# Kernel optimization log

Measured on AMD Instinct MI355X. Metric: run time of the kernel, lower is better.

Reference implementation:

```python
import jax, jax.numpy as jnp
import numpy as np

N, D, H, L = 50000, 128, 4, 3
E = 800000
C = D // H            # head dim = 32
NEG_SLOPE = 0.2       # PyG GATv2Conv default negative_slope
LN_EPS = 1e-5         # nn.LayerNorm default eps


def setup_inputs() -> dict:
    key = jax.random.key(0)
    ks = jax.random.split(key, 8)
    s = 1.0 / np.sqrt(D).astype(np.float32)
    return {
        "fine_poi_x": jax.random.normal(ks[0], (N, D), jnp.float32),
        "edge_index": jax.random.randint(ks[1], (2, E), 0, N, dtype=jnp.int32),
        "Wl": jax.random.normal(ks[2], (L, D, D), jnp.float32) * s,
        "bl": jnp.zeros((L, D), jnp.float32),
        "Wr": jax.random.normal(ks[3], (L, D, D), jnp.float32) * s,
        "br": jnp.zeros((L, D), jnp.float32),
        "att": jax.random.normal(ks[4], (L, H, C), jnp.float32) * s,
        "bias": jnp.zeros((L, D), jnp.float32),
        "gamma": jnp.ones((L, D), jnp.float32),
        "beta": jnp.zeros((L, D), jnp.float32),
    }


def _gatv2_conv(x, src, dst, Wl, bl, Wr, br, att, bias):
    # x: [N, D]; src/dst: [E'] (self-loops already appended)
    xl = (x @ Wl + bl).reshape(N, H, C)   # source-side transform (lin_l)
    xr = (x @ Wr + br).reshape(N, H, C)   # target-side transform (lin_r)
    m = xl[src] + xr[dst]                 # [E', H, C] per-edge pre-activation
    m = jax.nn.leaky_relu(m, NEG_SLOPE)
    e = jnp.einsum("ehc,hc->eh", m, att)  # [E', H] attention logits
    # segment softmax over edges grouped by destination node
    emax = jax.ops.segment_max(e, dst, num_segments=N)      # [N, H]
    ee = jnp.exp(e - emax[dst])
    denom = jax.ops.segment_sum(ee, dst, num_segments=N)    # [N, H]
    alpha = ee / denom[dst]               # self-loops guarantee denom >= 1 term
    out = jax.ops.segment_sum(xl[src] * alpha[:, :, None], dst, num_segments=N)
    return out.reshape(N, D) + bias


def _layernorm(x, g, b):
    mu = jnp.mean(x, axis=-1, keepdims=True)
    var = jnp.var(x, axis=-1, keepdims=True)
    return (x - mu) * jax.lax.rsqrt(var + LN_EPS) * g + b


def reference(fine_poi_x, edge_index, Wl, bl, Wr, br, att, bias, gamma, beta):
    # PyG GATv2Conv add_self_loops=True: append i->i edges
    loops = jnp.arange(N, dtype=edge_index.dtype)
    src = jnp.concatenate([edge_index[0], loops])
    dst = jnp.concatenate([edge_index[1], loops])
    x = fine_poi_x
    for i in range(L):
        h = _gatv2_conv(x, src, dst, Wl[i], bl[i], Wr[i], br[i], att[i], bias[i])
        x = _layernorm(x + h, gamma[i], beta[i])
        if i != L - 1:
            x = jax.nn.relu(x)
    return x
```

## Files before the change

### kernel.cpp

```cpp
#include <hip/hip_runtime.h>

#define N_NODES 50000
#define N_EDGES 800000
#define DIM 128
#define TOT_EDGES (N_EDGES + N_NODES)
#define LOG2E 1.44269504088896f

#define BSHIFT 9
#define BNODES 512
#define NB ((N_NODES + BNODES - 1) / BNODES)
#define BCAP 16384
#define EPB 4096
#define EPT 16
#define NBLK_A ((TOT_EDGES + EPB - 1) / EPB)

typedef __attribute__((ext_vector_type(8))) _Float16 f16x8;
typedef __attribute__((ext_vector_type(2))) _Float16 h2;
typedef __attribute__((ext_vector_type(4))) float f32x4;
typedef decltype(__builtin_amdgcn_cvt_pkrtz(0.f, 0.f)) fp16v2;

__device__ inline uint h2u(h2 v) { return __builtin_bit_cast(uint, v); }
__device__ inline h2 u2h(uint v) { return __builtin_bit_cast(h2, v); }
__device__ inline uint pk2u(fp16v2 v) { return __builtin_bit_cast(uint, v); }

__device__ inline float rowsum16(float v) {
  int x;
  x = __builtin_amdgcn_update_dpp(0, __float_as_int(v), 0x128, 0xF, 0xF, true);
  v += __int_as_float(x);
  x = __builtin_amdgcn_update_dpp(0, __float_as_int(v), 0x124, 0xF, 0xF, true);
  v += __int_as_float(x);
  x = __builtin_amdgcn_update_dpp(0, __float_as_int(v), 0x122, 0xF, 0xF, true);
  v += __int_as_float(x);
  x = __builtin_amdgcn_update_dpp(0, __float_as_int(v), 0x121, 0xF, 0xF, true);
  v += __int_as_float(x);
  return v;
}

__device__ inline float quadsum4(float v) {
  int x;
  x = __builtin_amdgcn_update_dpp(0, __float_as_int(v), 0xB1, 0xF, 0xF, true);
  v += __int_as_float(x);
  x = __builtin_amdgcn_update_dpp(0, __float_as_int(v), 0x4E, 0xF, 0xF, true);
  v += __int_as_float(x);
  return v;
}


__global__ __launch_bounds__(256) void convx_kernel(const float* __restrict__ x,
                                                    uint* __restrict__ xb,
                                                    int* __restrict__ bcnt) {
  if (blockIdx.x == 0 && threadIdx.x < NB) bcnt[threadIdx.x] = 0;
  int t = blockIdx.x * 256 + threadIdx.x;
  if (t < N_NODES * (DIM / 2)) {
    float2 v = ((const float2*)x)[t];
    xb[t] = pk2u(__builtin_amdgcn_cvt_pkrtz(v.x, v.y));
  }
}

__global__ __launch_bounds__(256) void convwa_kernel(const float* __restrict__ Wl,
                                                     const float* __restrict__ Wr,
                                                     ushort* __restrict__ Wt,
                                                     const float* __restrict__ att,
                                                     uint* __restrict__ attc,
                                                     uint* __restrict__ col) {
  int t = blockIdx.x * 256 + threadIdx.x;
  if (blockIdx.x == 0) {
    int u = threadIdx.x;
    if (u < 192) {
      float a0 = att[2 * u] * LOG2E, a1 = att[2 * u + 1] * LOG2E;
      attc[u] = pk2u(__builtin_amdgcn_cvt_pkrtz(a0, a1));
    }
    if (u < 64) col[TOT_EDGES + u] = 0u;
  }
  if (t >= 3 * 2 * DIM * DIM) return;
  int k = t & 127;
  int n = (t >> 7) & 127;
  int w = (t >> 14) & 1;
  int l = t >> 15;
  const float* W = w ? Wr : Wl;
  _Float16 h = (_Float16)W[l * DIM * DIM + k * DIM + n];
  Wt[t] = __builtin_bit_cast(ushort, h);
}


__global__ __launch_bounds__(256) void partA_kernel(const int* __restrict__ srcArr,
                                                    const int* __restrict__ dstArr,
                                                    int* __restrict__ bcnt,
                                                    uint2* __restrict__ bbuf) {
  int tid = threadIdx.x;
  int e0 = blockIdx.x * EPB;
  __shared__ int hist[NB], base[NB], loff[NB];
  if (tid < NB) { hist[tid] = 0; loff[tid] = 0; }
  __syncthreads();

  int sv[EPT], dv[EPT];
#pragma unroll
  for (int i = 0; i < EPT; ++i) {
    int e = e0 + i * 256 + tid;
    int s = 0, d = -1;
    if (e < TOT_EDGES) {
      if (e < N_EDGES) { s = srcArr[e]; d = dstArr[e]; }
      else { s = e - N_EDGES; d = s; }
    }
    sv[i] = s; dv[i] = d;
    if (d >= 0) atomicAdd(&hist[d >> BSHIFT], 1);
  }
  __syncthreads();
  if (tid < NB) {
    int h = hist[tid];
    if (h > 0) base[tid] = atomicAdd(&bcnt[tid], h);
  }
  __syncthreads();
#pragma unroll
  for (int i = 0; i < EPT; ++i) {
    int d = dv[i];
    if (d >= 0) {
      int b = d >> BSHIFT;
      int p = atomicAdd(&loff[b], 1);
      bbuf[(size_t)b * BCAP + base[b] + p] = make_uint2((uint)sv[i], (uint)d);
    }
  }
}


__global__ __launch_bounds__(512) void partB_kernel(const uint2* __restrict__ bbuf,
                                                    const int* __restrict__ bcnt,
                                                    int* __restrict__ rowptr,
                                                    uint* __restrict__ col) {
  int b = blockIdx.x, tid = threadIdx.x;

  __shared__ int s[128];
  if (tid < 128) s[tid] = (tid < NB) ? bcnt[tid] : 0;
  __syncthreads();
  for (int off = 1; off < 128; off <<= 1) {
    int t = 0;
    if (tid < 128 && tid >= off) t = s[tid - off];
    __syncthreads();
    if (tid < 128) s[tid] += t;
    __syncthreads();
  }
  int cb = (b > 0) ? s[b - 1] : 0;
  int m = bcnt[b];
  if (b == 0 && tid == 0) rowptr[N_NODES] = TOT_EDGES;
  const uint2* buf = bbuf + (size_t)b * BCAP;

  __shared__ int cnt[BNODES], scn[BNODES], cur[BNODES];
  cnt[tid] = 0;
  __syncthreads();
  for (int e = tid; e < m; e += 512) {
    int d = (int)buf[e].y;
    atomicAdd(&cnt[d & (BNODES - 1)], 1);
  }
  __syncthreads();
  int c = cnt[tid];
  scn[tid] = c;
  __syncthreads();
  for (int off = 1; off < BNODES; off <<= 1) {
    int t = (tid >= off) ? scn[tid - off] : 0;
    __syncthreads();
    scn[tid] += t;
    __syncthreads();
  }
  int excl = scn[tid] - c;
  int node = b * BNODES + tid;
  if (node < N_NODES) rowptr[node] = cb + excl;
  cur[tid] = excl;
  __syncthreads();
  for (int e = tid; e < m; e += 512) {
    uint2 sd = buf[e];
    int p = atomicAdd(&cur[(int)sd.y & (BNODES - 1)], 1);
    col[cb + p] = sd.x * 16u;
  }
}


__global__ __launch_bounds__(256) void gemm_mfma_kernel(
    const uint* __restrict__ xb,
    const ushort* __restrict__ Wt,
    const float* __restrict__ bl, const float* __restrict__ br,
    uint* __restrict__ xl, uint* __restrict__ xr) {
  int wave = threadIdx.x >> 6, lane = threadIdx.x & 63;
  int lr = lane & 15, kq = lane >> 4;
  int m0 = blockIdx.x * 64;

  const ushort* W = Wt + (wave >> 1) * (DIM * DIM);
  const float* bias = (wave >> 1) ? br : bl;
  uint* outp = (wave >> 1) ? xr : xl;
  int n0 = (wave & 1) * 64;
  const ushort* xbp = (const ushort*)xb;

  f16x8 bfrag[4][4];
#pragma unroll
  for (int nt = 0; nt < 4; ++nt)
#pragma unroll
    for (int kt = 0; kt < 4; ++kt)
      bfrag[nt][kt] = *(const f16x8*)(W + (n0 + nt * 16 + lr) * DIM + kt * 32 + kq * 8);

  f32x4 acc[4][4];
#pragma unroll
  for (int mt = 0; mt < 4; ++mt)
#pragma unroll
    for (int nt = 0; nt < 4; ++nt)
      acc[mt][nt] = (f32x4){0.f, 0.f, 0.f, 0.f};

  f16x8 af[4];
  {
    int m = m0 + lr;
    int mc = m < N_NODES ? m : N_NODES - 1;
#pragma unroll
    for (int kt = 0; kt < 4; ++kt)
      af[kt] = *(const f16x8*)(xbp + (size_t)mc * DIM + kt * 32 + kq * 8);
  }
#pragma unroll
  for (int mt = 0; mt < 4; ++mt) {
    f16x8 afn[4];
    if (mt < 3) {
      int m2 = m0 + (mt + 1) * 16 + lr;
      int mc2 = m2 < N_NODES ? m2 : N_NODES - 1;
#pragma unroll
      for (int kt = 0; kt < 4; ++kt)
        afn[kt] = *(const f16x8*)(xbp + (size_t)mc2 * DIM + kt * 32 + kq * 8);
    }
#pragma unroll
    for (int nt = 0; nt < 4; ++nt)
#pragma unroll
      for (int kt = 0; kt < 4; ++kt)
        acc[mt][nt] = __builtin_amdgcn_mfma_f32_16x16x32_f16(bfrag[nt][kt], af[kt],
                                                             acc[mt][nt], 0, 0, 0);
    if (mt < 3) {
      af[0] = afn[0]; af[1] = afn[1]; af[2] = afn[2]; af[3] = afn[3];
    }
  }

#pragma unroll
  for (int mt = 0; mt < 4; ++mt) {
    int m = m0 + mt * 16 + lr;
    if (m < N_NODES) {
#pragma unroll
      for (int nt = 0; nt < 4; ++nt) {
        int n = n0 + nt * 16 + kq * 4;
        float4 bb = *(const float4*)(bias + n);
        uint2 o;
        o.x = pk2u(__builtin_amdgcn_cvt_pkrtz(acc[mt][nt][0] + bb.x, acc[mt][nt][1] + bb.y));
        o.y = pk2u(__builtin_amdgcn_cvt_pkrtz(acc[mt][nt][2] + bb.z, acc[mt][nt][3] + bb.w));
        *(uint2*)(outp + (size_t)m * (DIM / 2) + (n >> 1)) = o;
      }
    }
  }
}


__global__ __launch_bounds__(64) void att_kernel(
    const uint4* __restrict__ xinb, const uint4* __restrict__ xlb,
    const uint4* __restrict__ xrb, const int* __restrict__ rowptr,
    const uint* __restrict__ col, const uint4* __restrict__ attc,
    const float4* __restrict__ bias, const float4* __restrict__ gamma,
    const float4* __restrict__ beta, uint4* __restrict__ xoutb,
    float4* __restrict__ xoutf, int do_relu) {
  int lane = threadIdx.x;
  uint j = (uint)(lane & 15);
  int e4 = lane >> 4;
  int n = blockIdx.x;

  uint4 rq = xrb[(uint)(n * 16) + j];
  uint4 aq = attc[j];
  h2 r2[4] = {u2h(rq.x), u2h(rq.y), u2h(rq.z), u2h(rq.w)};
  h2 at2[4] = {u2h(aq.x), u2h(aq.y), u2h(aq.z), u2h(aq.w)};
  const h2 c02 = {(_Float16)0.2f, (_Float16)0.2f};

  h2 accp[4] = {};
  float den = 0.f;

  int js = rowptr[n], je = rowptr[n + 1];

  uint cA = col[(uint)(js + e4)];
  uint cB = col[(uint)(js + 4 + e4)];
  uint cC = col[(uint)(js + 8 + e4)];
  uint4 gA = xlb[cA + j];
  uint4 gB = xlb[cB + j];

  for (int cbase = js; cbase < je; cbase += 4) {
    uint cD = col[(uint)(cbase + 12 + e4)];
    uint4 gC = xlb[cC + j];

    h2 a0 = u2h(gA.x), a1 = u2h(gA.y), a2 = u2h(gA.z), a3 = u2h(gA.w);
    float p = 0.f;
    {
      h2 s0 = a0 + r2[0], s1 = a1 + r2[1], s2 = a2 + r2[2], s3 = a3 + r2[3];
      h2 m0 = __builtin_elementwise_max(s0, s0 * c02);
      h2 m1 = __builtin_elementwise_max(s1, s1 * c02);
      h2 m2 = __builtin_elementwise_max(s2, s2 * c02);
      h2 m3 = __builtin_elementwise_max(s3, s3 * c02);
      p = __builtin_amdgcn_fdot2(__builtin_bit_cast(fp16v2, m0),
                                 __builtin_bit_cast(fp16v2, at2[0]), p, false);
      p = __builtin_amdgcn_fdot2(__builtin_bit_cast(fp16v2, m1),
                                 __builtin_bit_cast(fp16v2, at2[1]), p, false);
      p = __builtin_amdgcn_fdot2(__builtin_bit_cast(fp16v2, m2),
                                 __builtin_bit_cast(fp16v2, at2[2]), p, false);
      p = __builtin_amdgcn_fdot2(__builtin_bit_cast(fp16v2, m3),
                                 __builtin_bit_cast(fp16v2, at2[3]), p, false);
    }
    p = quadsum4(p);
    float w = (cbase + e4 < je) ? __builtin_amdgcn_exp2f(p) : 0.f;
    den += w;
    _Float16 wh = (_Float16)w;
    h2 w2 = {wh, wh};
    accp[0] = w2 * a0 + accp[0];
    accp[1] = w2 * a1 + accp[1];
    accp[2] = w2 * a2 + accp[2];
    accp[3] = w2 * a3 + accp[3];

    gA = gB; gB = gC; cC = cD;
  }

#pragma unroll
  for (int t = 0; t < 4; ++t) {
    accp[t] += u2h((uint)__shfl_xor((int)h2u(accp[t]), 16, 64));
    accp[t] += u2h((uint)__shfl_xor((int)h2u(accp[t]), 32, 64));
  }
  den += __shfl_xor(den, 16, 64);
  den += __shfl_xor(den, 32, 64);

  float inv = 1.0f / den;
  float acc[8];
#pragma unroll
  for (int t = 0; t < 4; ++t) {
    acc[2 * t] = (float)accp[t].x;
    acc[2 * t + 1] = (float)accp[t].y;
  }

  uint4 xi4 = xinb[(uint)(n * 16) + j];
  h2 xi[4] = {u2h(xi4.x), u2h(xi4.y), u2h(xi4.z), u2h(xi4.w)};
  float4 b0 = bias[2 * j], b1 = bias[2 * j + 1];

  float o[8];
  o[0] = fmaf(acc[0], inv, b0.x + (float)xi[0].x);
  o[1] = fmaf(acc[1], inv, b0.y + (float)xi[0].y);
  o[2] = fmaf(acc[2], inv, b0.z + (float)xi[1].x);
  o[3] = fmaf(acc[3], inv, b0.w + (float)xi[1].y);
  o[4] = fmaf(acc[4], inv, b1.x + (float)xi[2].x);
  o[5] = fmaf(acc[5], inv, b1.y + (float)xi[2].y);
  o[6] = fmaf(acc[6], inv, b1.z + (float)xi[3].x);
  o[7] = fmaf(acc[7], inv, b1.w + (float)xi[3].y);

  float s1 = 0.f, s2 = 0.f;
#pragma unroll
  for (int t = 0; t < 8; ++t) { s1 += o[t]; s2 = fmaf(o[t], o[t], s2); }
  s1 = rowsum16(s1);
  s2 = rowsum16(s2);
  float mean = s1 * (1.0f / DIM);
  float var = s2 * (1.0f / DIM) - mean * mean;
  float rstd = rsqrtf(var + 1e-5f);

  float4 g0 = gamma[2 * j], g1 = gamma[2 * j + 1];
  float4 t0 = beta[2 * j], t1 = beta[2 * j + 1];
  float y[8];
  y[0] = (o[0] - mean) * rstd * g0.x + t0.x;
  y[1] = (o[1] - mean) * rstd * g0.y + t0.y;
  y[2] = (o[2] - mean) * rstd * g0.z + t0.z;
  y[3] = (o[3] - mean) * rstd * g0.w + t0.w;
  y[4] = (o[4] - mean) * rstd * g1.x + t1.x;
  y[5] = (o[5] - mean) * rstd * g1.y + t1.y;
  y[6] = (o[6] - mean) * rstd * g1.z + t1.z;
  y[7] = (o[7] - mean) * rstd * g1.w + t1.w;
  if (do_relu) {
#pragma unroll
    for (int t = 0; t < 8; ++t) y[t] = fmaxf(y[t], 0.f);
  }

  if (e4 == 0) {
    if (xoutb) {
      uint4 ov;
      ov.x = pk2u(__builtin_amdgcn_cvt_pkrtz(y[0], y[1]));
      ov.y = pk2u(__builtin_amdgcn_cvt_pkrtz(y[2], y[3]));
      ov.z = pk2u(__builtin_amdgcn_cvt_pkrtz(y[4], y[5]));
      ov.w = pk2u(__builtin_amdgcn_cvt_pkrtz(y[6], y[7]));
      xoutb[(uint)(n * 16) + j] = ov;
    }
    if (xoutf) {
      xoutf[(uint)(n * 32) + 2 * j] = make_float4(y[0], y[1], y[2], y[3]);
      xoutf[(uint)(n * 32) + 2 * j + 1] = make_float4(y[4], y[5], y[6], y[7]);
    }
  }
}


extern "C" void kernel_launch(void* const* d_in, const int* in_sizes, int n_in,
                              void* d_out, int out_size, void* d_ws, size_t ws_size,
                              hipStream_t stream) {
  const float* x_in  = (const float*)d_in[0];
  const int*   eidx  = (const int*)d_in[1];
  const float* Wl    = (const float*)d_in[2];
  const float* bl    = (const float*)d_in[3];
  const float* Wr    = (const float*)d_in[4];
  const float* br    = (const float*)d_in[5];
  const float* att   = (const float*)d_in[6];
  const float* bias  = (const float*)d_in[7];
  const float* gamma = (const float*)d_in[8];
  const float* beta  = (const float*)d_in[9];
  float* out = (float*)d_out;

  char* p = (char*)d_ws;
  auto alloc = [&](size_t bytes) {
    char* q = p;
    p += (bytes + 255) & ~(size_t)255;
    return q;
  };
  uint*  xb       = (uint*)alloc((size_t)N_NODES * (DIM / 2) * 4);
  uint*  xlb      = (uint*)alloc((size_t)N_NODES * (DIM / 2) * 4);
  uint*  xrb      = (uint*)alloc((size_t)N_NODES * (DIM / 2) * 4);
  ushort* Wt      = (ushort*)alloc((size_t)3 * 2 * DIM * DIM * 2);
  uint*  attc     = (uint*)alloc((size_t)3 * 64 * 4);
  int*   rowptr   = (int*)alloc((size_t)(N_NODES + 1) * 4);
  uint*  col      = (uint*)alloc((size_t)(TOT_EDGES + 64) * 4);
  uint2* bbuf     = (uint2*)alloc((size_t)NB * BCAP * 8);
  int*   bcnt     = (int*)alloc((size_t)NB * 4);

  convx_kernel<<<(N_NODES * (DIM / 2) + 255) / 256, 256, 0, stream>>>(x_in, xb, bcnt);
  convwa_kernel<<<(3 * 2 * DIM * DIM + 255) / 256, 256, 0, stream>>>(Wl, Wr, Wt, att, attc, col);
  partA_kernel<<<NBLK_A, 256, 0, stream>>>(eidx, eidx + N_EDGES, bcnt, bbuf);
  partB_kernel<<<NB, 512, 0, stream>>>(bbuf, bcnt, rowptr, col);

  for (int l = 0; l < 3; ++l) {
    gemm_mfma_kernel<<<(N_NODES + 63) / 64, 256, 0, stream>>>(
        xb, Wt + (size_t)l * 2 * DIM * DIM, bl + l * DIM, br + l * DIM, xlb, xrb);
    att_kernel<<<N_NODES, 64, 0, stream>>>(
        (const uint4*)xb, (const uint4*)xlb, (const uint4*)xrb, rowptr, col,
        (const uint4*)(attc + l * 64), (const float4*)(bias + l * DIM),
        (const float4*)(gamma + l * DIM), (const float4*)(beta + l * DIM),
        (l == 2) ? nullptr : (uint4*)xb, (l == 2) ? (float4*)out : nullptr,
        (l != 2) ? 1 : 0);
  }
}
```

Before: 240.0 us.

## Pack bucket entries, shrink GEMM row tile, and run two nodes per attention block

Partition buckets now hold a single 32-bit word, source index shifted left by 9 bits OR'd with the low 9 bits of the destination, instead of a uint2 pair. This halves the bucket-buffer traffic in the CSR build. The GEMM kernel handles 32 rows per block instead of 64 and streams its B fragments from memory inside the loop rather than keeping a 4x4 array in registers. That cuts register use and doubles the block count, at the cost of reloading weights for each row tile. The attention kernel runs two waves per block, one node each, so half as many blocks are launched.

```diff
diff --git a/kernel.cpp b/kernel.cpp
--- a/kernel.cpp
+++ b/kernel.cpp
@@ -86,7 +86,7 @@
 __global__ __launch_bounds__(256) void partA_kernel(const int* __restrict__ srcArr,
                                                     const int* __restrict__ dstArr,
                                                     int* __restrict__ bcnt,
-                                                    uint2* __restrict__ bbuf) {
+                                                    uint* __restrict__ bbuf) {
   int tid = threadIdx.x;
   int e0 = blockIdx.x * EPB;
   __shared__ int hist[NB], base[NB], loff[NB];
@@ -117,13 +117,13 @@
     if (d >= 0) {
       int b = d >> BSHIFT;
       int p = atomicAdd(&loff[b], 1);
-      bbuf[(size_t)b * BCAP + base[b] + p] = make_uint2((uint)sv[i], (uint)d);
-    }
-  }
-}
-
-
-__global__ __launch_bounds__(512) void partB_kernel(const uint2* __restrict__ bbuf,
+      bbuf[(size_t)b * BCAP + base[b] + p] = ((uint)sv[i] << 9) | (uint)(d & (BNODES - 1));
+    }
+  }
+}
+
+
+__global__ __launch_bounds__(512) void partB_kernel(const uint* __restrict__ bbuf,
                                                     const int* __restrict__ bcnt,
                                                     int* __restrict__ rowptr,
                                                     uint* __restrict__ col) {
@@ -142,14 +142,13 @@
   int cb = (b > 0) ? s[b - 1] : 0;
   int m = bcnt[b];
   if (b == 0 && tid == 0) rowptr[N_NODES] = TOT_EDGES;
-  const uint2* buf = bbuf + (size_t)b * BCAP;
+  const uint* buf = bbuf + (size_t)b * BCAP;
 
   __shared__ int cnt[BNODES], scn[BNODES], cur[BNODES];
   cnt[tid] = 0;
   __syncthreads();
   for (int e = tid; e < m; e += 512) {
-    int d = (int)buf[e].y;
-    atomicAdd(&cnt[d & (BNODES - 1)], 1);
+    atomicAdd(&cnt[buf[e] & (BNODES - 1)], 1);
   }
   __syncthreads();
   int c = cnt[tid];
@@ -167,9 +166,9 @@
   cur[tid] = excl;
   __syncthreads();
   for (int e = tid; e < m; e += 512) {
-    uint2 sd = buf[e];
-    int p = atomicAdd(&cur[(int)sd.y & (BNODES - 1)], 1);
-    col[cb + p] = sd.x * 16u;
+    uint sd = buf[e];
+    int p = atomicAdd(&cur[sd & (BNODES - 1)], 1);
+    col[cb + p] = (sd >> 9) << 4;
   }
 }
 
@@ -181,7 +180,7 @@
     uint* __restrict__ xl, uint* __restrict__ xr) {
   int wave = threadIdx.x >> 6, lane = threadIdx.x & 63;
   int lr = lane & 15, kq = lane >> 4;
-  int m0 = blockIdx.x * 64;
+  int m0 = blockIdx.x * 32;
 
   const ushort* W = Wt + (wave >> 1) * (DIM * DIM);
   const float* bias = (wave >> 1) ? br : bl;
@@ -189,16 +188,9 @@
   int n0 = (wave & 1) * 64;
   const ushort* xbp = (const ushort*)xb;
 
-  f16x8 bfrag[4][4];
-#pragma unroll
-  for (int nt = 0; nt < 4; ++nt)
-#pragma unroll
-    for (int kt = 0; kt < 4; ++kt)
-      bfrag[nt][kt] = *(const f16x8*)(W + (n0 + nt * 16 + lr) * DIM + kt * 32 + kq * 8);
-
-  f32x4 acc[4][4];
-#pragma unroll
-  for (int mt = 0; mt < 4; ++mt)
+  f32x4 acc[2][4];
+#pragma unroll
+  for (int mt = 0; mt < 2; ++mt)
 #pragma unroll
     for (int nt = 0; nt < 4; ++nt)
       acc[mt][nt] = (f32x4){0.f, 0.f, 0.f, 0.f};
@@ -212,28 +204,33 @@
       af[kt] = *(const f16x8*)(xbp + (size_t)mc * DIM + kt * 32 + kq * 8);
   }
 #pragma unroll
-  for (int mt = 0; mt < 4; ++mt) {
+  for (int mt = 0; mt < 2; ++mt) {
     f16x8 afn[4];
-    if (mt < 3) {
-      int m2 = m0 + (mt + 1) * 16 + lr;
+    if (mt < 1) {
+      int m2 = m0 + 16 + lr;
       int mc2 = m2 < N_NODES ? m2 : N_NODES - 1;
 #pragma unroll
       for (int kt = 0; kt < 4; ++kt)
         afn[kt] = *(const f16x8*)(xbp + (size_t)mc2 * DIM + kt * 32 + kq * 8);
     }
 #pragma unroll
-    for (int nt = 0; nt < 4; ++nt)
+    for (int nt = 0; nt < 4; ++nt) {
+      f16x8 bf[4];
 #pragma unroll
       for (int kt = 0; kt < 4; ++kt)
-        acc[mt][nt] = __builtin_amdgcn_mfma_f32_16x16x32_f16(bfrag[nt][kt], af[kt],
+        bf[kt] = *(const f16x8*)(W + (n0 + nt * 16 + lr) * DIM + kt * 32 + kq * 8);
+#pragma unroll
+      for (int kt = 0; kt < 4; ++kt)
+        acc[mt][nt] = __builtin_amdgcn_mfma_f32_16x16x32_f16(bf[kt], af[kt],
                                                              acc[mt][nt], 0, 0, 0);
-    if (mt < 3) {
+    }
+    if (mt < 1) {
       af[0] = afn[0]; af[1] = afn[1]; af[2] = afn[2]; af[3] = afn[3];
     }
   }
 
 #pragma unroll
-  for (int mt = 0; mt < 4; ++mt) {
+  for (int mt = 0; mt < 2; ++mt) {
     int m = m0 + mt * 16 + lr;
     if (m < N_NODES) {
 #pragma unroll
@@ -250,17 +247,17 @@
 }
 
 
-__global__ __launch_bounds__(64) void att_kernel(
+__global__ __launch_bounds__(128) void att_kernel(
     const uint4* __restrict__ xinb, const uint4* __restrict__ xlb,
     const uint4* __restrict__ xrb, const int* __restrict__ rowptr,
     const uint* __restrict__ col, const uint4* __restrict__ attc,
     const float4* __restrict__ bias, const float4* __restrict__ gamma,
     const float4* __restrict__ beta, uint4* __restrict__ xoutb,
     float4* __restrict__ xoutf, int do_relu) {
-  int lane = threadIdx.x;
+  int lane = threadIdx.x & 63;
   uint j = (uint)(lane & 15);
   int e4 = lane >> 4;
-  int n = blockIdx.x;
+  int n = blockIdx.x * 2 + (threadIdx.x >> 6);
 
   uint4 rq = xrb[(uint)(n * 16) + j];
   uint4 aq = attc[j];
@@ -413,7 +410,7 @@
   uint*  attc     = (uint*)alloc((size_t)3 * 64 * 4);
   int*   rowptr   = (int*)alloc((size_t)(N_NODES + 1) * 4);
   uint*  col      = (uint*)alloc((size_t)(TOT_EDGES + 64) * 4);
-  uint2* bbuf     = (uint2*)alloc((size_t)NB * BCAP * 8);
+  uint*  bbuf     = (uint*)alloc((size_t)NB * BCAP * 4);
   int*   bcnt     = (int*)alloc((size_t)NB * 4);
 
   convx_kernel<<<(N_NODES * (DIM / 2) + 255) / 256, 256, 0, stream>>>(x_in, xb, bcnt);
@@ -422,9 +419,9 @@
   partB_kernel<<<NB, 512, 0, stream>>>(bbuf, bcnt, rowptr, col);
 
   for (int l = 0; l < 3; ++l) {
-    gemm_mfma_kernel<<<(N_NODES + 63) / 64, 256, 0, stream>>>(
+    gemm_mfma_kernel<<<(N_NODES + 31) / 32, 256, 0, stream>>>(
         xb, Wt + (size_t)l * 2 * DIM * DIM, bl + l * DIM, br + l * DIM, xlb, xrb);
-    att_kernel<<<N_NODES, 64, 0, stream>>>(
+    att_kernel<<<N_NODES / 2, 128, 0, stream>>>(
         (const uint4*)xb, (const uint4*)xlb, (const uint4*)xrb, rowptr, col,
         (const uint4*)(attc + l * 64), (const float4*)(bias + l * DIM),
         (const float4*)(gamma + l * DIM), (const float4*)(beta + l * DIM),
```

Result: slower. 252.6 us (+5.3%).
